# Kernel optimization log

Measured on AMD Instinct MI355X. Metric: run time of the kernel, lower is better.

Reference implementation:

```python
import jax, jax.numpy as jnp
import numpy as np

WIN = (2, 6, 12)            # (win_pl, win_lat, win_lon)
RES = (8, 48, 360)          # (pl, lat, lon) input resolution
DIM = 192
HEADS = 6
TOW = (RES[0] // WIN[0]) * (RES[1] // WIN[1])   # type_of_windows = 32
NLON = RES[2] // WIN[2]                          # 30
N = WIN[0] * WIN[1] * WIN[2]                     # 144
TABLE = WIN[0] ** 2 * WIN[1] ** 2 * (2 * WIN[2] - 1)  # 3312


def _earth_position_index():
    wp, wl, ww = WIN
    zi = np.arange(wp); zj = -np.arange(wp) * wp
    hi = np.arange(wl); hj = -np.arange(wl) * wl
    w = np.arange(ww)
    c1 = np.stack(np.meshgrid(zi, hi, w, indexing='ij')).reshape(3, -1)
    c2 = np.stack(np.meshgrid(zj, hj, w, indexing='ij')).reshape(3, -1)
    coords = (c1[:, :, None] - c2[:, None, :]).transpose(1, 2, 0).copy()
    coords[:, :, 2] += ww - 1
    coords[:, :, 1] *= 2 * ww - 1
    coords[:, :, 0] *= (2 * ww - 1) * wl * wl
    return coords.sum(-1).astype(np.int32)  # (N, N)


def setup_inputs() -> dict:
    key = jax.random.key(0)
    ks = jax.random.split(key, 5)
    B_ = NLON  # batch 1 * num_lon
    x = jax.random.normal(ks[0], (B_, TOW, N, DIM), dtype=jnp.float32)
    mask = jnp.zeros((NLON, TOW, N, N), dtype=jnp.float32)
    qkv_w = jax.random.normal(ks[1], (3 * DIM, DIM), dtype=jnp.float32) * 0.02
    qkv_b = jnp.zeros((3 * DIM,), dtype=jnp.float32)
    proj_w = jax.random.normal(ks[2], (DIM, DIM), dtype=jnp.float32) * 0.02
    proj_b = jnp.zeros((DIM,), dtype=jnp.float32)
    bias_table = jax.random.normal(ks[3], (TABLE, TOW, HEADS), dtype=jnp.float32) * 0.02
    pos_index = jnp.asarray(_earth_position_index())
    return {"x": x, "mask": mask, "qkv_w": qkv_w, "qkv_b": qkv_b,
            "proj_w": proj_w, "proj_b": proj_b, "bias_table": bias_table,
            "pos_index": pos_index}


def reference(x, mask, qkv_w, qkv_b, proj_w, proj_b, bias_table, pos_index):
    B_, nW, Nn, C = x.shape
    H = HEADS
    hd = C // H
    scale = hd ** (-0.5)
    # QKV projection -> (3, B_, H, nW, N, hd)
    qkv = (x @ qkv_w.T + qkv_b).reshape(B_, nW, Nn, 3, H, hd)
    qkv = qkv.transpose(3, 0, 4, 1, 2, 5)
    q, k, v = qkv[0], qkv[1], qkv[2]
    # attention scores (B_, H, nW, N, N)
    attn = jnp.einsum('bhwnd,bhwmd->bhwnm', q * scale, k)
    # earth position bias: gather then (H, nW, N, N)
    bias = bias_table[pos_index.reshape(-1)].reshape(Nn, Nn, nW, H)
    bias = bias.transpose(3, 2, 0, 1)
    attn = attn + bias[None]
    # mask add: view B_ as (B, nLon)
    nLon = mask.shape[0]
    attn = attn.reshape(B_ // nLon, nLon, H, nW, Nn, Nn) + mask[None, :, None]
    attn = attn.reshape(B_, H, nW, Nn, Nn)
    attn = jax.nn.softmax(attn, axis=-1)
    # weighted values -> (B_, nW, N, C)
    out = jnp.einsum('bhwnm,bhwmd->bwnhd', attn, v).reshape(B_, nW, Nn, C)
    out = out @ proj_w.T + proj_b
    return out
```

## Files before the change

kernel.cpp:

```cpp
#include <hip/hip_runtime.h>
#include <hip/hip_bf16.h>

#define DIM    192
#define HEADS  6
#define HD     32
#define NTOK   144
#define NWIN   960
#define NBWH   (NWIN * HEADS)
#define TOKENS (NWIN * NTOK)
#define PPITCH 168
#define XPITCH 200
#define NTILE  (TOKENS / 32)
#define QKV_GRID  512
#define PROJ_GRID 1024
#define LOG2E  1.4426950408889634f

typedef __attribute__((ext_vector_type(8))) short bf16x8;
typedef __attribute__((ext_vector_type(4))) float f32x4;
typedef __attribute__((ext_vector_type(4))) short short4v;

static __device__ __forceinline__ short f2bf(float f) {
  __hip_bfloat16 h = __float2bfloat16(f);
  return __builtin_bit_cast(short, h);
}
static __device__ __forceinline__ float bf2f(short s) {
  unsigned u = ((unsigned)(unsigned short)s) << 16;
  return __builtin_bit_cast(float, u);
}

#define NBIAS (32 * HEADS * NTOK * NTOK)
#define NMASK (NWIN * NTOK * NTOK)
#define NWQ   (3 * DIM * DIM)
#define NWP   (DIM * DIM)
#define NWQ8  (NWQ / 8)
#define NWP8  (NWP / 8)
#define PRPITCH 148
#define NWH   (32 * HEADS)
#define PREP_GRID (NWIN + NWH + 72)

__global__ __launch_bounds__(256) void prep_kernel(
    const float* __restrict__ qkv_w, const float* __restrict__ proj_w,
    const float* __restrict__ bias_table, const int* __restrict__ pos_index,
    const float* __restrict__ mask,
    short* __restrict__ wq_b, short* __restrict__ wp_b,
    short* __restrict__ biasT, short* __restrict__ maskT)
{
  __shared__ __align__(16) short tile[NTOK * PRPITCH];
  const int blk = blockIdx.x;
  const int t   = threadIdx.x;

  if (blk < NWIN) {
    const int bw = blk;
    const float* mrow = mask + (size_t)bw * NTOK * NTOK;
    for (int idx = t; idx < (NTOK * NTOK) / 4; idx += 256) {
      int qq = idx / (NTOK / 4);
      int k4 = (idx - qq * (NTOK / 4)) * 4;
      float4 f = *(const float4*)(mrow + qq * NTOK + k4);
      short4v o4;
      o4[0] = f2bf(f.x * LOG2E); o4[1] = f2bf(f.y * LOG2E);
      o4[2] = f2bf(f.z * LOG2E); o4[3] = f2bf(f.w * LOG2E);
      *(short4v*)(tile + qq * PRPITCH + k4) = o4;
    }
    __syncthreads();
    short* outp = maskT + (size_t)bw * (9 * NTOK * 16);
    for (int c = t; c < 9 * NTOK * 2; c += 256) {
      int q8  = c & 1;
      int kqt = c >> 1;
      int k   = kqt % NTOK;
      int qt  = kqt / NTOK;
      int q0  = qt * 16 + q8 * 8;
      bf16x8 o;
#pragma unroll
      for (int j = 0; j < 8; ++j) o[j] = tile[(q0 + j) * PRPITCH + k];
      *(bf16x8*)(outp + c * 8) = o;
    }
  } else if (blk < NWIN + NWH) {
    const int wh = blk - NWIN;
    for (int idx = t; idx < (NTOK * NTOK) / 4; idx += 256) {
      int qq = idx / (NTOK / 4);
      int k4 = (idx - qq * (NTOK / 4)) * 4;
      int4 p = *(const int4*)(pos_index + qq * NTOK + k4);
      short4v o4;
      o4[0] = f2bf(bias_table[(size_t)p.x * NWH + wh] * LOG2E);
      o4[1] = f2bf(bias_table[(size_t)p.y * NWH + wh] * LOG2E);
      o4[2] = f2bf(bias_table[(size_t)p.z * NWH + wh] * LOG2E);
      o4[3] = f2bf(bias_table[(size_t)p.w * NWH + wh] * LOG2E);
      *(short4v*)(tile + qq * PRPITCH + k4) = o4;
    }
    __syncthreads();
    short* outp = biasT + (size_t)wh * (9 * NTOK * 16);
    for (int c = t; c < 9 * NTOK * 2; c += 256) {
      int q8  = c & 1;
      int kqt = c >> 1;
      int k   = kqt % NTOK;
      int qt  = kqt / NTOK;
      int q0  = qt * 16 + q8 * 8;
      bf16x8 o;
#pragma unroll
      for (int j = 0; j < 8; ++j) o[j] = tile[(q0 + j) * PRPITCH + k];
      *(bf16x8*)(outp + c * 8) = o;
    }
  } else {
    int j = (blk - NWIN - NWH) * 256 + t;
    if (j < NWQ8) {
      int flat = j * 8;
      float4 f0 = *(const float4*)(qkv_w + flat);
      float4 f1 = *(const float4*)(qkv_w + flat + 4);
      bf16x8 o;
      o[0]=f2bf(f0.x); o[1]=f2bf(f0.y); o[2]=f2bf(f0.z); o[3]=f2bf(f0.w);
      o[4]=f2bf(f1.x); o[5]=f2bf(f1.y); o[6]=f2bf(f1.z); o[7]=f2bf(f1.w);
      *(bf16x8*)(wq_b + flat) = o;
    } else if (j < NWQ8 + NWP8) {
      int flat = (j - NWQ8) * 8;
      float4 f0 = *(const float4*)(proj_w + flat);
      float4 f1 = *(const float4*)(proj_w + flat + 4);
      bf16x8 o;
      o[0]=f2bf(f0.x); o[1]=f2bf(f0.y); o[2]=f2bf(f0.z); o[3]=f2bf(f0.w);
      o[4]=f2bf(f1.x); o[5]=f2bf(f1.y); o[6]=f2bf(f1.z); o[7]=f2bf(f1.w);
      *(bf16x8*)(wp_b + flat) = o;
    }
  }
}

__global__ __launch_bounds__(768, 3) void qkv_gemm(
    const float* __restrict__ x, const short* __restrict__ wq,
    const float* __restrict__ qbias,
    short* __restrict__ q, short* __restrict__ k, short* __restrict__ v)
{
  __shared__ __align__(16) short xs[2][32 * XPITCH];

  const int wave = threadIdx.x >> 6, lane = threadIdx.x & 63;
  const int m = lane & 15, g = lane >> 4;
  const int c0w = wave * 48;

  bf16x8 wfrag[3][6];
#pragma unroll
  for (int ct = 0; ct < 3; ++ct)
#pragma unroll
    for (int ks = 0; ks < 6; ++ks)
      wfrag[ct][ks] = *(const bf16x8*)(wq + (size_t)(c0w + ct * 16 + m) * DIM + ks * 32 + g * 8);

  const int which = wave >> 2;
  short* dst = which == 0 ? q : (which == 1 ? k : v);
  const float sc = which == 0 ? (0.17677669529663689f * LOG2E) : 1.0f;

  float4 b4[3];
  int hh[3], d0[3];
#pragma unroll
  for (int ct = 0; ct < 3; ++ct) {
    int co0 = c0w + ct * 16 + g * 4;
    b4[ct] = *(const float4*)(qbias + co0);
    int rem = co0 - which * DIM;
    hh[ct] = rem >> 5; d0[ct] = rem & 31;
  }

  const int srow = threadIdx.x / 24;
  const int scg  = threadIdx.x % 24;

  {
    const float* xp = x + ((size_t)(blockIdx.x * 32 + srow)) * DIM + scg * 8;
    float4 f0 = ((const float4*)xp)[0];
    float4 f1 = ((const float4*)xp)[1];
    bf16x8 o;
    o[0]=f2bf(f0.x); o[1]=f2bf(f0.y); o[2]=f2bf(f0.z); o[3]=f2bf(f0.w);
    o[4]=f2bf(f1.x); o[5]=f2bf(f1.y); o[6]=f2bf(f1.z); o[7]=f2bf(f1.w);
    *(bf16x8*)(&xs[0][srow * XPITCH + scg * 8]) = o;
  }
  __syncthreads();

  int cur = 0;
  for (int t = blockIdx.x; t < NTILE; t += QKV_GRID) {
    const int tn = t + QKV_GRID;
    const bool have = tn < NTILE;
    float4 f0, f1;
    if (have) {
      const float* xp = x + ((size_t)(tn * 32 + srow)) * DIM + scg * 8;
      f0 = ((const float4*)xp)[0];
      f1 = ((const float4*)xp)[1];
    }

    f32x4 acc[3][2];
#pragma unroll
    for (int ct = 0; ct < 3; ++ct)
#pragma unroll
      for (int rt = 0; rt < 2; ++rt) acc[ct][rt] = (f32x4){0.f, 0.f, 0.f, 0.f};

#pragma unroll
    for (int ks = 0; ks < 6; ++ks) {
      const short* bp_ = &xs[cur][m * XPITCH + ks * 32 + g * 8];
      bf16x8 b0 = *(const bf16x8*)bp_;
      bf16x8 b1 = *(const bf16x8*)(bp_ + 16 * XPITCH);
#pragma unroll
      for (int ct = 0; ct < 3; ++ct) {
        acc[ct][0] = __builtin_amdgcn_mfma_f32_16x16x32_bf16(wfrag[ct][ks], b0, acc[ct][0], 0, 0, 0);
        acc[ct][1] = __builtin_amdgcn_mfma_f32_16x16x32_bf16(wfrag[ct][ks], b1, acc[ct][1], 0, 0, 0);
      }
    }

#pragma unroll
    for (int ct = 0; ct < 3; ++ct) {
#pragma unroll
      for (int rt = 0; rt < 2; ++rt) {
        int tok = t * 32 + rt * 16 + m;
        int bw = tok / NTOK, n = tok - bw * NTOK;
        short4v s;
        s[0] = f2bf((acc[ct][rt][0] + b4[ct].x) * sc);
        s[1] = f2bf((acc[ct][rt][1] + b4[ct].y) * sc);
        s[2] = f2bf((acc[ct][rt][2] + b4[ct].z) * sc);
        s[3] = f2bf((acc[ct][rt][3] + b4[ct].w) * sc);
        *(short4v*)(dst + ((size_t)(bw * HEADS + hh[ct]) * NTOK + n) * HD + d0[ct]) = s;
      }
    }

    if (have) {
      bf16x8 o;
      o[0]=f2bf(f0.x); o[1]=f2bf(f0.y); o[2]=f2bf(f0.z); o[3]=f2bf(f0.w);
      o[4]=f2bf(f1.x); o[5]=f2bf(f1.y); o[6]=f2bf(f1.z); o[7]=f2bf(f1.w);
      *(bf16x8*)(&xs[cur ^ 1][srow * XPITCH + scg * 8]) = o;
    }
    __syncthreads();
    cur ^= 1;
  }
}

__global__ __launch_bounds__(192, 3) void attn_kernel(
    const short* __restrict__ q, const short* __restrict__ k,
    const short* __restrict__ v, const short* __restrict__ biasT,
    const short* __restrict__ maskT, short* __restrict__ aout)
{
  const int b    = blockIdx.x;
  const int xcd  = b & 7;
  const int slot = b >> 3;
  const int bw   = xcd * 120 + slot / 6;
  const int h    = slot % 6;
  const int bwh  = bw * HEADS + h;
  const int w    = bw & 31;

  __shared__ __align__(16) short kls[NTOK * HD];
  __shared__ __align__(16) short vt[HD * PPITCH];
  __shared__ __align__(16) short pl[3 * 16 * PPITCH];

  const size_t base = (size_t)bwh * (NTOK * HD);
  const short* qb = q + base;
  const short* kb = k + base;
  const short* vb = v + base;

  for (int i = threadIdx.x; i < (NTOK * HD) / 8; i += 192) {
    *(bf16x8*)(kls + i * 8) = *(const bf16x8*)(kb + i * 8);
    int n = i >> 2, dg = (i & 3) * 8;
    bf16x8 vv = *(const bf16x8*)(vb + n * HD + dg);
#pragma unroll
    for (int j = 0; j < 8; ++j) vt[(dg + j) * PPITCH + n] = vv[j];
  }
  for (int i = threadIdx.x; i < 128; i += 192) {
    int d = i >> 2, c = 144 + (i & 3) * 4;
    *(short4v*)&vt[d * PPITCH + c] = (short4v){0, 0, 0, 0};
  }
  __syncthreads();

  const int wv = threadIdx.x >> 6;
  const int lane = threadIdx.x & 63;
  const int m = lane & 15, g = lane >> 4;
  short* myp = pl + wv * 16 * PPITCH;
  {
    int r = lane >> 2, c = 144 + (lane & 3) * 4;
    *(short4v*)&myp[r * PPITCH + c] = (short4v){0, 0, 0, 0};
  }

  const short* bp = biasT + (size_t)(w * HEADS + h) * (9 * NTOK * 16);
  const short* mp = maskT + (size_t)bw * (9 * NTOK * 16);

  for (int rt = wv * 3; rt < wv * 3 + 3; ++rt) {
    const int i0 = rt * 16;
    const short* bpt = bp + rt * (NTOK * 16);
    const short* mpt = mp + rt * (NTOK * 16);
    bf16x8 aq = *(const bf16x8*)(qb + (size_t)(i0 + m) * HD + g * 8);
    f32x4 s[9];
#pragma unroll
    for (int jt = 0; jt < 9; ++jt) {
      const int key = jt * 16 + m;
      short4v bb = *(const short4v*)(bpt + key * 16 + g * 4);
      short4v mm = *(const short4v*)(mpt + key * 16 + g * 4);
      f32x4 cini;
#pragma unroll
      for (int r = 0; r < 4; ++r) cini[r] = bf2f(bb[r]) + bf2f(mm[r]);
      bf16x8 bk = *(const bf16x8*)(kls + key * HD + g * 8);
      s[jt] = __builtin_amdgcn_mfma_f32_16x16x32_bf16(aq, bk, cini, 0, 0, 0);
    }
    float sum[4] = {0.f, 0.f, 0.f, 0.f};
#pragma unroll
    for (int jt = 0; jt < 9; ++jt) {
#pragma unroll
      for (int r = 0; r < 4; ++r) {
        float e = __builtin_amdgcn_exp2f(s[jt][r]);
        s[jt][r] = e;
        sum[r] += e;
      }
    }
#pragma unroll
    for (int r = 0; r < 4; ++r) {
      sum[r] += __shfl_xor(sum[r], 1, 64);
      sum[r] += __shfl_xor(sum[r], 2, 64);
      sum[r] += __shfl_xor(sum[r], 4, 64);
      sum[r] += __shfl_xor(sum[r], 8, 64);
    }
    float rs[4];
#pragma unroll
    for (int r = 0; r < 4; ++r) rs[r] = 1.0f / sum[r];
#pragma unroll
    for (int jt = 0; jt < 9; ++jt)
#pragma unroll
      for (int r = 0; r < 4; ++r)
        myp[(g * 4 + r) * PPITCH + jt * 16 + m] = f2bf(s[jt][r]);

    float xs0 = (lane & 1) ? rs[1] : rs[0];
    float xs1 = (lane & 1) ? rs[3] : rs[2];
    float xsel = (lane & 2) ? xs1 : xs0;
    float rv = __shfl(xsel, ((m >> 2) << 4) | (m & 3), 64);

    f32x4 o0 = (f32x4){0.f, 0.f, 0.f, 0.f};
    f32x4 o1 = (f32x4){0.f, 0.f, 0.f, 0.f};
#pragma unroll
    for (int kt = 0; kt < 5; ++kt) {
      bf16x8 ap = *(const bf16x8*)(myp + m * PPITCH + kt * 32 + g * 8);
      bf16x8 b0 = *(const bf16x8*)(vt + m * PPITCH + kt * 32 + g * 8);
      bf16x8 b1 = *(const bf16x8*)(vt + (16 + m) * PPITCH + kt * 32 + g * 8);
      o0 = __builtin_amdgcn_mfma_f32_16x16x32_bf16(b0, ap, o0, 0, 0, 0);
      o1 = __builtin_amdgcn_mfma_f32_16x16x32_bf16(b1, ap, o1, 0, 0, 0);
    }
    size_t ob = ((size_t)(bw * NTOK + i0 + m)) * DIM + h * HD + g * 4;
    short4v s0, s1;
#pragma unroll
    for (int r = 0; r < 4; ++r) { s0[r] = f2bf(o0[r] * rv); s1[r] = f2bf(o1[r] * rv); }
    *(short4v*)(aout + ob) = s0;
    *(short4v*)(aout + ob + 16) = s1;
  }
}

__global__ __launch_bounds__(256, 3) void proj_gemm(
    const short* __restrict__ ain, const short* __restrict__ pw,
    const float* __restrict__ pb, float* __restrict__ out)
{
  __shared__ __align__(16) short as_[2][32 * XPITCH];

  const int wave = threadIdx.x >> 6, lane = threadIdx.x & 63;
  const int m = lane & 15, g = lane >> 4;
  const int c0w = wave * 48;

  bf16x8 wfrag[3][6];
#pragma unroll
  for (int ct = 0; ct < 3; ++ct)
#pragma unroll
    for (int ks = 0; ks < 6; ++ks)
      wfrag[ct][ks] = *(const bf16x8*)(pw + (size_t)(c0w + ct * 16 + m) * DIM + ks * 32 + g * 8);

  float4 b4[3];
#pragma unroll
  for (int ct = 0; ct < 3; ++ct)
    b4[ct] = *(const float4*)(pb + c0w + ct * 16 + g * 4);

  const int srow = threadIdx.x >> 3;
  const int scg  = threadIdx.x & 7;

  {
    const short* sp = ain + ((size_t)(blockIdx.x * 32 + srow)) * DIM + scg * 24;
    short* dp = &as_[0][srow * XPITCH + scg * 24];
#pragma unroll
    for (int i = 0; i < 3; ++i)
      *(bf16x8*)(dp + i * 8) = *(const bf16x8*)(sp + i * 8);
  }
  __syncthreads();

  int cur = 0;
  for (int t = blockIdx.x; t < NTILE; t += PROJ_GRID) {
    const int tn = t + PROJ_GRID;
    const bool have = tn < NTILE;
    bf16x8 r0, r1, r2;
    if (have) {
      const short* sp = ain + ((size_t)(tn * 32 + srow)) * DIM + scg * 24;
      r0 = *(const bf16x8*)(sp);
      r1 = *(const bf16x8*)(sp + 8);
      r2 = *(const bf16x8*)(sp + 16);
    }

    f32x4 acc[3][2];
#pragma unroll
    for (int ct = 0; ct < 3; ++ct)
#pragma unroll
      for (int rt = 0; rt < 2; ++rt) acc[ct][rt] = (f32x4){0.f, 0.f, 0.f, 0.f};

#pragma unroll
    for (int ks = 0; ks < 6; ++ks) {
      const short* bp_ = &as_[cur][m * XPITCH + ks * 32 + g * 8];
      bf16x8 b0 = *(const bf16x8*)bp_;
      bf16x8 b1 = *(const bf16x8*)(bp_ + 16 * XPITCH);
#pragma unroll
      for (int ct = 0; ct < 3; ++ct) {
        acc[ct][0] = __builtin_amdgcn_mfma_f32_16x16x32_bf16(wfrag[ct][ks], b0, acc[ct][0], 0, 0, 0);
        acc[ct][1] = __builtin_amdgcn_mfma_f32_16x16x32_bf16(wfrag[ct][ks], b1, acc[ct][1], 0, 0, 0);
      }
    }

#pragma unroll
    for (int ct = 0; ct < 3; ++ct) {
      int co0 = c0w + ct * 16 + g * 4;
#pragma unroll
      for (int rt = 0; rt < 2; ++rt) {
        int tok = t * 32 + rt * 16 + m;
        float4 o;
        o.x = acc[ct][rt][0] + b4[ct].x;
        o.y = acc[ct][rt][1] + b4[ct].y;
        o.z = acc[ct][rt][2] + b4[ct].z;
        o.w = acc[ct][rt][3] + b4[ct].w;
        *(float4*)(out + (size_t)tok * DIM + co0) = o;
      }
    }

    if (have) {
      short* dp = &as_[cur ^ 1][srow * XPITCH + scg * 24];
      *(bf16x8*)(dp)      = r0;
      *(bf16x8*)(dp + 8)  = r1;
      *(bf16x8*)(dp + 16) = r2;
    }
    __syncthreads();
    cur ^= 1;
  }
}

extern "C" void kernel_launch(void* const* d_in, const int* in_sizes, int n_in,
                              void* d_out, int out_size, void* d_ws, size_t ws_size,
                              hipStream_t stream) {
  const float* x          = (const float*)d_in[0];
  const float* mask       = (const float*)d_in[1];
  const float* qkv_w      = (const float*)d_in[2];
  const float* qkv_b      = (const float*)d_in[3];
  const float* proj_w     = (const float*)d_in[4];
  const float* proj_b     = (const float*)d_in[5];
  const float* bias_table = (const float*)d_in[6];
  const int*   pos_index  = (const int*)d_in[7];
  float* out = (float*)d_out;

  const size_t NELEM = (size_t)TOKENS * DIM;
  short* qv    = (short*)d_ws;
  short* kv    = qv + NELEM;
  short* vv    = kv + NELEM;
  short* aout  = vv + NELEM;
  short* wqb   = aout + NELEM;
  short* wpb   = wqb + NWQ;
  short* biasT = wpb + NWP;
  short* maskT = biasT + NBIAS;

  prep_kernel<<<PREP_GRID, 256, 0, stream>>>(
      qkv_w, proj_w, bias_table, pos_index, mask, wqb, wpb, biasT, maskT);
  qkv_gemm<<<QKV_GRID, 768, 0, stream>>>(x, wqb, qkv_b, qv, kv, vv);
  attn_kernel<<<NBWH, 192, 0, stream>>>(qv, kv, vv, biasT, maskT, aout);
  proj_gemm<<<PROJ_GRID, 256, 0, stream>>>(aout, wpb, proj_b, out);
}
```

Measured before the change: 431.6 us.

## Deepen QKV prefetch, pad K/V LDS pitches, split attention launch in two

The QKV GEMM now prefetches x two tiles ahead in registers instead of one, to hide global load latency. In the attention kernel, K is stored in LDS with a padded row pitch of 36 and the P/V pitch drops from 168 to 164, both meant to cut bank conflicts on row reads. The attention grid is also split into two half launches using a block offset. That split adds launch overhead and a tail between the halves, and the odd padding may misalign 16-byte vector LDS accesses.

```diff
diff --git a/kernel.cpp b/kernel.cpp
--- a/kernel.cpp
+++ b/kernel.cpp
@@ -8,7 +8,8 @@
 #define NWIN   960
 #define NBWH   (NWIN * HEADS)
 #define TOKENS (NWIN * NTOK)
-#define PPITCH 168
+#define PPITCH 164
+#define KPITCH 36
 #define XPITCH 200
 #define NTILE  (TOKENS / 32)
 #define QKV_GRID  512
@@ -166,17 +167,22 @@
     o[4]=f2bf(f1.x); o[5]=f2bf(f1.y); o[6]=f2bf(f1.z); o[7]=f2bf(f1.w);
     *(bf16x8*)(&xs[0][srow * XPITCH + scg * 8]) = o;
   }
+  float4 a0 = (float4){0,0,0,0}, a1 = (float4){0,0,0,0};
+  if (blockIdx.x + QKV_GRID < NTILE) {
+    const float* xp = x + ((size_t)((blockIdx.x + QKV_GRID) * 32 + srow)) * DIM + scg * 8;
+    a0 = ((const float4*)xp)[0];
+    a1 = ((const float4*)xp)[1];
+  }
   __syncthreads();
 
   int cur = 0;
   for (int t = blockIdx.x; t < NTILE; t += QKV_GRID) {
-    const int tn = t + QKV_GRID;
-    const bool have = tn < NTILE;
-    float4 f0, f1;
-    if (have) {
-      const float* xp = x + ((size_t)(tn * 32 + srow)) * DIM + scg * 8;
-      f0 = ((const float4*)xp)[0];
-      f1 = ((const float4*)xp)[1];
+    const bool haveB = (t + 2 * QKV_GRID) < NTILE;
+    float4 n0 = (float4){0,0,0,0}, n1 = (float4){0,0,0,0};
+    if (haveB) {
+      const float* xp = x + ((size_t)((t + 2 * QKV_GRID) * 32 + srow)) * DIM + scg * 8;
+      n0 = ((const float4*)xp)[0];
+      n1 = ((const float4*)xp)[1];
     }
 
     f32x4 acc[3][2];
@@ -212,23 +218,24 @@
       }
     }
 
-    if (have) {
+    if (t + QKV_GRID < NTILE) {
       bf16x8 o;
-      o[0]=f2bf(f0.x); o[1]=f2bf(f0.y); o[2]=f2bf(f0.z); o[3]=f2bf(f0.w);
-      o[4]=f2bf(f1.x); o[5]=f2bf(f1.y); o[6]=f2bf(f1.z); o[7]=f2bf(f1.w);
+      o[0]=f2bf(a0.x); o[1]=f2bf(a0.y); o[2]=f2bf(a0.z); o[3]=f2bf(a0.w);
+      o[4]=f2bf(a1.x); o[5]=f2bf(a1.y); o[6]=f2bf(a1.z); o[7]=f2bf(a1.w);
       *(bf16x8*)(&xs[cur ^ 1][srow * XPITCH + scg * 8]) = o;
     }
     __syncthreads();
     cur ^= 1;
+    a0 = n0; a1 = n1;
   }
 }
 
 __global__ __launch_bounds__(192, 3) void attn_kernel(
     const short* __restrict__ q, const short* __restrict__ k,
     const short* __restrict__ v, const short* __restrict__ biasT,
-    const short* __restrict__ maskT, short* __restrict__ aout)
+    const short* __restrict__ maskT, short* __restrict__ aout, int bbase)
 {
-  const int b    = blockIdx.x;
+  const int b    = blockIdx.x + bbase;
   const int xcd  = b & 7;
   const int slot = b >> 3;
   const int bw   = xcd * 120 + slot / 6;
@@ -236,7 +243,7 @@
   const int bwh  = bw * HEADS + h;
   const int w    = bw & 31;
 
-  __shared__ __align__(16) short kls[NTOK * HD];
+  __shared__ __align__(16) short kls[NTOK * KPITCH];
   __shared__ __align__(16) short vt[HD * PPITCH];
   __shared__ __align__(16) short pl[3 * 16 * PPITCH];
 
@@ -246,8 +253,8 @@
   const short* vb = v + base;
 
   for (int i = threadIdx.x; i < (NTOK * HD) / 8; i += 192) {
-    *(bf16x8*)(kls + i * 8) = *(const bf16x8*)(kb + i * 8);
     int n = i >> 2, dg = (i & 3) * 8;
+    *(bf16x8*)(kls + n * KPITCH + dg) = *(const bf16x8*)(kb + i * 8);
     bf16x8 vv = *(const bf16x8*)(vb + n * HD + dg);
 #pragma unroll
     for (int j = 0; j < 8; ++j) vt[(dg + j) * PPITCH + n] = vv[j];
@@ -284,7 +291,7 @@
       f32x4 cini;
 #pragma unroll
       for (int r = 0; r < 4; ++r) cini[r] = bf2f(bb[r]) + bf2f(mm[r]);
-      bf16x8 bk = *(const bf16x8*)(kls + key * HD + g * 8);
+      bf16x8 bk = *(const bf16x8*)(kls + key * KPITCH + g * 8);
       s[jt] = __builtin_amdgcn_mfma_f32_16x16x32_bf16(aq, bk, cini, 0, 0, 0);
     }
     float sum[4] = {0.f, 0.f, 0.f, 0.f};
@@ -453,6 +460,7 @@
   prep_kernel<<<PREP_GRID, 256, 0, stream>>>(
       qkv_w, proj_w, bias_table, pos_index, mask, wqb, wpb, biasT, maskT);
   qkv_gemm<<<QKV_GRID, 768, 0, stream>>>(x, wqb, qkv_b, qv, kv, vv);
-  attn_kernel<<<NBWH, 192, 0, stream>>>(qv, kv, vv, biasT, maskT, aout);
+  attn_kernel<<<NBWH / 2, 192, 0, stream>>>(qv, kv, vv, biasT, maskT, aout, 0);
+  attn_kernel<<<NBWH / 2, 192, 0, stream>>>(qv, kv, vv, biasT, maskT, aout, NBWH / 2);
   proj_gemm<<<PROJ_GRID, 256, 0, stream>>>(aout, wpb, proj_b, out);
 }
```

New measurement: 443.9 us. 1.03x slower.
